# Performance work log

Measured on AMD Instinct MI355X. Metric: run time of the kernel, lower is better.

The kernel has to match this reference:

```python
import jax, jax.numpy as jnp
import numpy as np

N, C, H, W = 8, 512, 56, 56
CI = 256  # inter_channels = in_channels // reduction


def setup_inputs() -> dict:
    key = jax.random.key(0)
    ks = jax.random.split(key, 9)
    std = 0.01
    return {
        "x": jax.random.normal(ks[0], (N, C, H, W), dtype=jnp.float32),
        "W_g": jax.random.normal(ks[1], (CI, C), dtype=jnp.float32) * std,
        "b_g": jnp.zeros((CI,), dtype=jnp.float32),
        "W_theta": jax.random.normal(ks[2], (CI, C), dtype=jnp.float32) * std,
        "b_theta": jnp.zeros((CI,), dtype=jnp.float32),
        "W_phi": jax.random.normal(ks[3], (CI, C), dtype=jnp.float32) * std,
        "b_phi": jnp.zeros((CI,), dtype=jnp.float32),
        "W_out": jax.random.normal(ks[4], (C, CI), dtype=jnp.float32) * std,
        "b_out": jax.random.normal(ks[5], (C,), dtype=jnp.float32) * std,
    }


def _proj(Wt, b, xf):
    # 1x1 conv == channel GEMM over flattened spatial positions: (n, o, L)
    return jnp.einsum('oc,ncl->nol', Wt, xf) + b[None, :, None]


def reference(x, W_g, b_g, W_theta, b_theta, W_phi, b_phi, W_out, b_out):
    n, c, h, w = x.shape
    L = h * w
    xf = x.reshape(n, c, L)

    g_x = _proj(W_g, b_g, xf).transpose(0, 2, 1)          # (n, L, ci)
    theta_x = _proj(W_theta, b_theta, xf).transpose(0, 2, 1)  # (n, L, ci)
    phi_x = _proj(W_phi, b_phi, xf)                        # (n, ci, L)

    ci = theta_x.shape[-1]
    # embedded_gaussian with use_scale=True
    pairwise = jnp.einsum('nqc,nck->nqk', theta_x, phi_x) / jnp.sqrt(
        jnp.asarray(ci, dtype=x.dtype))
    pairwise = jax.nn.softmax(pairwise, axis=-1)           # (n, L, L)

    y = jnp.einsum('nqk,nkc->nqc', pairwise, g_x)          # (n, L, ci)
    y = y.transpose(0, 2, 1)                               # (n, ci, L)
    out = _proj(W_out, b_out, y).reshape(n, c, h, w)
    return x + out
```

## Files before the change

kernel.cpp:

```cpp
#include <hip/hip_runtime.h>
#include <stdint.h>

#define NB 8
#define CC 512
#define LL 3136
#define CIN 256

typedef __attribute__((ext_vector_type(8))) short bf8;
typedef __attribute__((ext_vector_type(4))) float f4;
typedef __attribute__((ext_vector_type(16))) float f16v;

__device__ __forceinline__ f4 mfma_bf16(bf8 a, bf8 b, f4 c) {
  return __builtin_amdgcn_mfma_f32_16x16x32_bf16(a, b, c, 0, 0, 0);
}

__device__ __forceinline__ f16v mfma32(bf8 a, bf8 b, f16v c) {
  return __builtin_amdgcn_mfma_f32_32x32x16_bf16(a, b, c, 0, 0, 0);
}

__device__ __forceinline__ unsigned short f2bf(float f) {
  unsigned int u = __float_as_uint(f);
  u += 0x7FFFu + ((u >> 16) & 1u);
  return (unsigned short)(u >> 16);
}

__device__ __forceinline__ void gload_lds16(const unsigned short* g, unsigned short* l) {
  __builtin_amdgcn_global_load_lds(
      (const __attribute__((address_space(1))) void*)g,
      (__attribute__((address_space(3))) void*)l, 16, 0, 0);
}

__global__ void k_convw(const float* Wth, const float* Wph, const float* Wg, const float* Wout,
                        unsigned short* dst) {
  int i = blockIdx.x * 256 + threadIdx.x;
  int which = i >> 17;
  int off = i & 131071;
  const float* s = which == 0 ? Wth : which == 1 ? Wph : which == 2 ? Wg : Wout;
  dst[i] = f2bf(s[off]);
}

__global__ __launch_bounds__(256) void k_xT(const float* x, unsigned short* xT) {
  __shared__ unsigned short tile[64][66];
  const int lt = blockIdx.x, n = blockIdx.y, ct = blockIdx.z;
  const int t = threadIdx.x;
  const float* xb = x + (size_t)n * CC * LL + (size_t)(ct * 64) * LL + lt * 64;
  const int tl = t & 63, trow = t >> 6;
#pragma unroll
  for (int i = 0; i < 16; ++i) {
    int c = i * 4 + trow;
    tile[c][tl] = f2bf(xb[(size_t)c * LL + tl]);
  }
  __syncthreads();
  unsigned short* xo = xT + (size_t)n * LL * CC + (size_t)(lt * 64) * CC + ct * 64;
  const int tc = t & 63, lrow = t >> 6;
#pragma unroll
  for (int i = 0; i < 16; ++i) {
    int l = i * 4 + lrow;
    xo[(size_t)l * CC + tc] = tile[tc][l];
  }
}

__global__ __launch_bounds__(256, 3) void k_proj(const unsigned short* Wbf,
    const float* bth, const float* bph, const float* bg,
    const unsigned short* xT, unsigned short* QT, unsigned short* KT, unsigned short* Vb) {
  __shared__ unsigned short wtile[2][8192];
  __shared__ unsigned short xtile[2][4096];
  const int bid = blockIdx.x;
  const int n = bid & 7, t = bid >> 3;
  const int lt = t % 49, z = t / 49;
  const int proj = z >> 1, cith = z & 1;
  const int tid = threadIdx.x;
  const int wave = tid >> 6, lane = tid & 63;
  const int quad = lane >> 4, c16 = lane & 15;

  const unsigned short* Wg = Wbf + proj * 131072 + (size_t)(cith * 128) * CC;
  const unsigned short* Xg = xT + (size_t)n * LL * CC + (size_t)(lt * 64) * CC;

  auto issue = [&](int chunk, int b) {
    const int cb = chunk * 64;
#pragma unroll
    for (int i = 0; i < 4; ++i) {
      int seg = i * 4 + wave;
      int p = seg * 64 + lane;
      int r = p >> 3, sl = p & 7, g = sl ^ (r & 7);
      gload_lds16(Wg + (size_t)r * CC + cb + g * 8, &wtile[b][seg * 512]);
    }
#pragma unroll
    for (int i = 0; i < 2; ++i) {
      int seg = i * 4 + wave;
      int p = seg * 64 + lane;
      int r = p >> 3, sl = p & 7, g = sl ^ (r & 7);
      gload_lds16(Xg + (size_t)r * CC + cb + g * 8, &xtile[b][seg * 512]);
    }
  };

  const f4 zz = {0.f, 0.f, 0.f, 0.f};
  f4 acc[2][4];
#pragma unroll
  for (int i = 0; i < 2; ++i)
#pragma unroll
    for (int j = 0; j < 4; ++j) acc[i][j] = zz;

  issue(0, 0);
  for (int chunk = 0; chunk < 8; ++chunk) {
    __syncthreads();
    if (chunk + 1 < 8) issue(chunk + 1, (chunk + 1) & 1);
    const int bb = chunk & 1;
#pragma unroll
    for (int kc = 0; kc < 2; ++kc) {
      const int slot = (kc * 4 + quad) ^ (c16 & 7);
      bf8 wf[2], xf[4];
#pragma unroll
      for (int sub = 0; sub < 2; ++sub)
        wf[sub] = *(const bf8*)(&wtile[bb][(wave * 32 + sub * 16 + c16) * 64 + slot * 8]);
#pragma unroll
      for (int nt = 0; nt < 4; ++nt)
        xf[nt] = *(const bf8*)(&xtile[bb][(nt * 16 + c16) * 64 + slot * 8]);
      if (proj < 2) {
#pragma unroll
        for (int sub = 0; sub < 2; ++sub)
#pragma unroll
          for (int nt = 0; nt < 4; ++nt)
            acc[sub][nt] = mfma_bf16(wf[sub], xf[nt], acc[sub][nt]);
      } else {
#pragma unroll
        for (int sub = 0; sub < 2; ++sub)
#pragma unroll
          for (int nt = 0; nt < 4; ++nt)
            acc[sub][nt] = mfma_bf16(xf[nt], wf[sub], acc[sub][nt]);
      }
    }
  }

  if (proj < 2) {
    const float* bias = proj == 0 ? bth : bph;
    unsigned short* dst = proj == 0 ? QT : KT;
#pragma unroll
    for (int sub = 0; sub < 2; ++sub) {
      const int ciB = cith * 128 + wave * 32 + sub * 16 + quad * 4;
      const float b0 = bias[ciB + 0], b1 = bias[ciB + 1];
      const float b2 = bias[ciB + 2], b3 = bias[ciB + 3];
#pragma unroll
      for (int nt = 0; nt < 4; ++nt) {
        int l = lt * 64 + nt * 16 + c16;
        ushort4 v;
        v.x = f2bf(acc[sub][nt][0] + b0);
        v.y = f2bf(acc[sub][nt][1] + b1);
        v.z = f2bf(acc[sub][nt][2] + b2);
        v.w = f2bf(acc[sub][nt][3] + b3);
        *(ushort4*)(dst + ((size_t)n * LL + l) * CIN + ciB) = v;
      }
    }
  } else {
#pragma unroll
    for (int sub = 0; sub < 2; ++sub) {
      const int ci = cith * 128 + wave * 32 + sub * 16 + c16;
      const float bv = bg[ci];
#pragma unroll
      for (int nt = 0; nt < 4; ++nt) {
        int l = lt * 64 + nt * 16 + quad * 4;
        ushort4 v;
        v.x = f2bf(acc[sub][nt][0] + bv);
        v.y = f2bf(acc[sub][nt][1] + bv);
        v.z = f2bf(acc[sub][nt][2] + bv);
        v.w = f2bf(acc[sub][nt][3] + bv);
        *(ushort4*)(Vb + ((size_t)n * CIN + ci) * LL + l) = v;
      }
    }
  }
}

__global__ __launch_bounds__(256, 2) void k_attn(const unsigned short* QT, const unsigned short* KT,
                                                 const unsigned short* Vb, unsigned short* Opart,
                                                 float* denp) {
  __shared__ unsigned short kbuf[2][8192];
  __shared__ unsigned short vbuf[2][8192];
  __shared__ __align__(16) unsigned short plds[4][1280];
  const int bid = blockIdx.x;
  const int n = bid & 7, ks = (bid >> 3) & 1, qb = bid >> 4;
  const int tid = threadIdx.x;
  const int wave = tid >> 6, lane = tid & 63;
  const int l31 = lane & 31, half = lane >> 5;
  int q0 = qb * 128 + wave * 32;
  const bool do_store = q0 < LL;
  if (q0 > LL - 32) q0 = LL - 32;
  const unsigned short* Qb = QT + ((size_t)n * LL + q0) * CIN;
  const unsigned short* Kks = KT + (size_t)n * LL * CIN + (size_t)(ks * 49 * 32) * CIN;
  const unsigned short* Vks = Vb + (size_t)n * CIN * LL + ks * 49 * 32;

  const float qs = 0.09016844005556021f;
  bf8 qf[16];
#pragma unroll
  for (int kc = 0; kc < 16; ++kc) {
    bf8 q = *(const bf8*)(Qb + (size_t)l31 * CIN + kc * 16 + half * 8);
#pragma unroll
    for (int e = 0; e < 8; ++e) {
      float f = __uint_as_float(((unsigned)(unsigned short)q[e]) << 16) * qs;
      q[e] = (short)f2bf(f);
    }
    qf[kc] = q;
  }

  f16v o[8];
#pragma unroll
  for (int t = 0; t < 8; ++t)
#pragma unroll
    for (int r = 0; r < 16; ++r) o[t][r] = 0.f;
  float sden = 0.f;

  auto issue = [&](int kt, int b) {
    const int k0 = kt * 32;
    const unsigned short* Kg = Kks + (size_t)k0 * CIN;
    const unsigned short* Vg = Vks + k0;
#pragma unroll
    for (int i = 0; i < 4; ++i) {
      int seg = i * 4 + wave;
      int idx = seg * 64 + lane;
      {
        int r = idx >> 5, sl = idx & 31, g = sl ^ r;
        gload_lds16(Kg + r * CIN + g * 8, &kbuf[b][seg * 512]);
      }
      {
        int r = idx >> 2, sl = idx & 3, g = sl ^ ((r >> 1) & 3);
        gload_lds16(Vg + (size_t)r * LL + g * 8, &vbuf[b][seg * 512]);
      }
    }
  };

  unsigned short* pw = &plds[wave][0];
  issue(0, 0);
  for (int kt = 0; kt < 49; ++kt) {
    __syncthreads();
    if (kt + 1 < 49) issue(kt + 1, (kt + 1) & 1);
    const int b = kt & 1;
    const unsigned short* kb = &kbuf[b][0];
    const unsigned short* vbp = &vbuf[b][0];

    f16v sc;
#pragma unroll
    for (int r = 0; r < 16; ++r) sc[r] = 0.f;
#pragma unroll
    for (int kc = 0; kc < 16; ++kc) {
      int slot = (kc * 2 + half) ^ l31;
      bf8 bfr = *(const bf8*)(kb + l31 * 256 + slot * 8);
      sc = mfma32(qf[kc], bfr, sc);
    }
#pragma unroll
    for (int r = 0; r < 16; ++r) {
      float p = __builtin_amdgcn_exp2f(sc[r]);
      int row = (r & 3) + 8 * (r >> 2) + 4 * half;
      pw[row * 40 + l31] = f2bf(p);
    }
    bf8 af[2];
#pragma unroll
    for (int kc2 = 0; kc2 < 2; ++kc2) {
      af[kc2] = *(const bf8*)(pw + l31 * 40 + kc2 * 16 + half * 8);
#pragma unroll
      for (int e = 0; e < 8; ++e)
        sden += __uint_as_float(((unsigned)(unsigned short)af[kc2][e]) << 16);
    }
#pragma unroll
    for (int t = 0; t < 8; ++t) {
#pragma unroll
      for (int kc2 = 0; kc2 < 2; ++kc2) {
        int slot = (kc2 * 2 + half) ^ ((l31 >> 1) & 3);
        bf8 v = *(const bf8*)(vbp + (t * 32 + l31) * 32 + slot * 8);
        o[t] = mfma32(af[kc2], v, o[t]);
      }
    }
  }

  sden += __shfl_xor(sden, 32);

  if (do_store) {
    if (lane < 32) denp[((size_t)ks * NB + n) * LL + q0 + l31] = sden;
    unsigned short* Ob = Opart + (((size_t)ks * NB + n) * LL + q0) * CIN;
#pragma unroll
    for (int t = 0; t < 8; ++t)
#pragma unroll
      for (int r = 0; r < 16; ++r) {
        int row = (r & 3) + 8 * (r >> 2) + 4 * half;
        Ob[(size_t)row * CIN + t * 32 + l31] = f2bf(o[t][r]);
      }
  }
}

__global__ void k_den(const float* denp, float* invden) {
  int i = blockIdx.x * 256 + threadIdx.x;
  if (i < NB * LL) invden[i] = 1.f / (denp[i] + denp[NB * LL + i]);
}

__global__ __launch_bounds__(256, 3) void k_out(const unsigned short* O0, const unsigned short* O1,
    const unsigned short* Wo, const float* bout, const float* invden,
    const float* x, float* out) {
  __shared__ unsigned short wtile[2][8192];
  __shared__ unsigned short otile[2][4096];
  const int bid = blockIdx.x;
  const int n = bid & 7, t = bid >> 3;
  const int lt = t % 49, cth = t / 49;
  const int tid = threadIdx.x;
  const int wave = tid >> 6, lane = tid & 63;
  const int quad = lane >> 4, c16 = lane & 15;

  const unsigned short* Wg = Wo + (size_t)(cth * 128) * CIN;
  const unsigned short* Og0 = O0 + ((size_t)n * LL + lt * 64) * CIN;
  const unsigned short* Og1 = O1 + ((size_t)n * LL + lt * 64) * CIN;

  auto issue = [&](int chunk, int b) {
    const int cb = (chunk & 3) * 64;
    const unsigned short* Og = chunk < 4 ? Og0 : Og1;
#pragma unroll
    for (int i = 0; i < 4; ++i) {
      int seg = i * 4 + wave;
      int p = seg * 64 + lane;
      int r = p >> 3, sl = p & 7, g = sl ^ (r & 7);
      gload_lds16(Wg + (size_t)r * CIN + cb + g * 8, &wtile[b][seg * 512]);
    }
#pragma unroll
    for (int i = 0; i < 2; ++i) {
      int seg = i * 4 + wave;
      int p = seg * 64 + lane;
      int r = p >> 3, sl = p & 7, g = sl ^ (r & 7);
      gload_lds16(Og + (size_t)r * CIN + cb + g * 8, &otile[b][seg * 512]);
    }
  };

  const f4 zz = {0.f, 0.f, 0.f, 0.f};
  f4 acc[4][2];
#pragma unroll
  for (int i = 0; i < 4; ++i)
#pragma unroll
    for (int j = 0; j < 2; ++j) acc[i][j] = zz;

  issue(0, 0);
  for (int chunk = 0; chunk < 8; ++chunk) {
    __syncthreads();
    if (chunk + 1 < 8) issue(chunk + 1, (chunk + 1) & 1);
    const int bb = chunk & 1;
#pragma unroll
    for (int kc = 0; kc < 2; ++kc) {
      const int slot = (kc * 4 + quad) ^ (c16 & 7);
      bf8 wf[2], ofr[4];
#pragma unroll
      for (int sub = 0; sub < 2; ++sub)
        wf[sub] = *(const bf8*)(&wtile[bb][(wave * 32 + sub * 16 + c16) * 64 + slot * 8]);
#pragma unroll
      for (int nt = 0; nt < 4; ++nt)
        ofr[nt] = *(const bf8*)(&otile[bb][(nt * 16 + c16) * 64 + slot * 8]);
#pragma unroll
      for (int nt = 0; nt < 4; ++nt)
#pragma unroll
        for (int sub = 0; sub < 2; ++sub)
          acc[nt][sub] = mfma_bf16(ofr[nt], wf[sub], acc[nt][sub]);
    }
  }

#pragma unroll
  for (int sub = 0; sub < 2; ++sub) {
    const int c = cth * 128 + wave * 32 + sub * 16 + c16;
    const float bv = bout[c];
#pragma unroll
    for (int nt = 0; nt < 4; ++nt) {
      int l = lt * 64 + nt * 16 + quad * 4;
      f4 iv = *(const f4*)(invden + (size_t)n * LL + l);
      size_t base = ((size_t)n * CC + c) * LL + l;
      f4 xv = *(const f4*)(x + base);
      f4 r;
      r[0] = xv[0] + bv + acc[nt][sub][0] * iv[0];
      r[1] = xv[1] + bv + acc[nt][sub][1] * iv[1];
      r[2] = xv[2] + bv + acc[nt][sub][2] * iv[2];
      r[3] = xv[3] + bv + acc[nt][sub][3] * iv[3];
      *(f4*)(out + base) = r;
    }
  }
}

extern "C" void kernel_launch(void* const* d_in, const int* in_sizes, int n_in,
                              void* d_out, int out_size, void* d_ws, size_t ws_size,
                              hipStream_t stream) {
  const float* x     = (const float*)d_in[0];
  const float* W_g   = (const float*)d_in[1];
  const float* b_g   = (const float*)d_in[2];
  const float* W_th  = (const float*)d_in[3];
  const float* b_th  = (const float*)d_in[4];
  const float* W_ph  = (const float*)d_in[5];
  const float* b_ph  = (const float*)d_in[6];
  const float* W_out = (const float*)d_in[7];
  const float* b_out = (const float*)d_in[8];

  char* ws = (char*)d_ws;
  const size_t SZ_W  = 1048576;
  const size_t SZ_P  = 12845056;
  unsigned short* Wbf = (unsigned short*)(ws);
  unsigned short* QT  = (unsigned short*)(ws + SZ_W);
  unsigned short* KT  = (unsigned short*)(ws + SZ_W + SZ_P);
  unsigned short* Vb  = (unsigned short*)(ws + SZ_W + 2 * SZ_P);
  unsigned short* xT  = (unsigned short*)(ws + SZ_W + 3 * SZ_P);
  unsigned short* O0  = xT;
  unsigned short* O1  = (unsigned short*)(ws + SZ_W + 4 * SZ_P);
  float* denp   = (float*)(ws + SZ_W + 5 * SZ_P);
  float* invden = (float*)(ws + SZ_W + 5 * SZ_P + 2 * NB * LL * 4);
  float* out = (float*)d_out;

  k_convw<<<2048, 256, 0, stream>>>(W_th, W_ph, W_g, W_out, Wbf);
  k_xT<<<dim3(49, 8, 8), 256, 0, stream>>>(x, xT);
  k_proj<<<2352, 256, 0, stream>>>(Wbf, b_th, b_ph, b_g, xT, QT, KT, Vb);
  k_attn<<<400, 256, 0, stream>>>(QT, KT, Vb, O0, denp);
  k_den<<<98, 256, 0, stream>>>(denp, invden);
  k_out<<<1568, 256, 0, stream>>>(O0, O1, Wbf + 3 * 131072, b_out, invden, x, out);
}
```

Before: 306.3 us.

## Compute S^T and build P operand in registers via permlane32 swap, dropping LDS staging

The QK^T MFMA now takes the operands in swapped order, so scores come out transposed, and the accumulation is split across two independent accumulators to shorten the MFMA dependency chain. The exp values are packed to bf16 with v_cvt_pk_bf16_f32, and v_permlane32_swap rearranges them directly into the A-operand layout for the PV MFMA. This removes the per-tile LDS write/read round trip of P and the per-wave plds buffer. The row-sum denominator is now taken from the fp32 probabilities rather than the bf16-rounded ones, which slightly changes the numerics.

Measured after the change: 335.1 us. 1.09x slower.

```diff
diff --git a/kernel.cpp b/kernel.cpp
--- a/kernel.cpp
+++ b/kernel.cpp
@@ -9,6 +9,7 @@
 typedef __attribute__((ext_vector_type(8))) short bf8;
 typedef __attribute__((ext_vector_type(4))) float f4;
 typedef __attribute__((ext_vector_type(16))) float f16v;
+typedef __attribute__((ext_vector_type(4))) int i4;
 
 __device__ __forceinline__ f4 mfma_bf16(bf8 a, bf8 b, f4 c) {
   return __builtin_amdgcn_mfma_f32_16x16x32_bf16(a, b, c, 0, 0, 0);
@@ -22,6 +23,12 @@
   unsigned int u = __float_as_uint(f);
   u += 0x7FFFu + ((u >> 16) & 1u);
   return (unsigned short)(u >> 16);
+}
+
+__device__ __forceinline__ int cvtpk_bf16(float lo, float hi) {
+  int r;
+  asm("v_cvt_pk_bf16_f32 %0, %1, %2" : "=v"(r) : "v"(lo), "v"(hi));
+  return r;
 }
 
 __device__ __forceinline__ void gload_lds16(const unsigned short* g, unsigned short* l) {
@@ -175,7 +182,6 @@
                                                  float* denp) {
   __shared__ unsigned short kbuf[2][8192];
   __shared__ unsigned short vbuf[2][8192];
-  __shared__ __align__(16) unsigned short plds[4][1280];
   const int bid = blockIdx.x;
   const int n = bid & 7, ks = (bid >> 3) & 1, qb = bid >> 4;
   const int tid = threadIdx.x;
@@ -227,7 +233,6 @@
     }
   };
 
-  unsigned short* pw = &plds[wave][0];
   issue(0, 0);
   for (int kt = 0; kt < 49; ++kt) {
     __syncthreads();
@@ -236,29 +241,45 @@
     const unsigned short* kb = &kbuf[b][0];
     const unsigned short* vbp = &vbuf[b][0];
 
-    f16v sc;
-#pragma unroll
-    for (int r = 0; r < 16; ++r) sc[r] = 0.f;
-#pragma unroll
-    for (int kc = 0; kc < 16; ++kc) {
-      int slot = (kc * 2 + half) ^ l31;
-      bf8 bfr = *(const bf8*)(kb + l31 * 256 + slot * 8);
-      sc = mfma32(qf[kc], bfr, sc);
-    }
-#pragma unroll
-    for (int r = 0; r < 16; ++r) {
-      float p = __builtin_amdgcn_exp2f(sc[r]);
-      int row = (r & 3) + 8 * (r >> 2) + 4 * half;
-      pw[row * 40 + l31] = f2bf(p);
-    }
+    f16v sc0, sc1;
+#pragma unroll
+    for (int r = 0; r < 16; ++r) { sc0[r] = 0.f; sc1[r] = 0.f; }
+#pragma unroll
+    for (int kc = 0; kc < 16; kc += 2) {
+      int slot0 = (kc * 2 + half) ^ l31;
+      int slot1 = ((kc + 1) * 2 + half) ^ l31;
+      bf8 kf0 = *(const bf8*)(kb + l31 * 256 + slot0 * 8);
+      bf8 kf1 = *(const bf8*)(kb + l31 * 256 + slot1 * 8);
+      sc0 = mfma32(kf0, qf[kc], sc0);
+      sc1 = mfma32(kf1, qf[kc + 1], sc1);
+    }
+
+    float p[16];
+#pragma unroll
+    for (int r = 0; r < 16; ++r)
+      p[r] = __builtin_amdgcn_exp2f(sc0[r] + sc1[r]);
+    {
+      float s0 = (p[0] + p[1]) + (p[2] + p[3]);
+      float s1 = (p[4] + p[5]) + (p[6] + p[7]);
+      float s2 = (p[8] + p[9]) + (p[10] + p[11]);
+      float s3 = (p[12] + p[13]) + (p[14] + p[15]);
+      sden += (s0 + s1) + (s2 + s3);
+    }
+
     bf8 af[2];
 #pragma unroll
-    for (int kc2 = 0; kc2 < 2; ++kc2) {
-      af[kc2] = *(const bf8*)(pw + l31 * 40 + kc2 * 16 + half * 8);
-#pragma unroll
-      for (int e = 0; e < 8; ++e)
-        sden += __uint_as_float(((unsigned)(unsigned short)af[kc2][e]) << 16);
-    }
+    for (int m = 0; m < 2; ++m) {
+      int x0 = cvtpk_bf16(p[8 * m + 0], p[8 * m + 1]);
+      int y0 = cvtpk_bf16(p[8 * m + 4], p[8 * m + 5]);
+      int x1 = cvtpk_bf16(p[8 * m + 2], p[8 * m + 3]);
+      int y1 = cvtpk_bf16(p[8 * m + 6], p[8 * m + 7]);
+      asm("v_permlane32_swap_b32 %0, %1" : "+v"(x0), "+v"(y0));
+      asm("v_permlane32_swap_b32 %0, %1" : "+v"(x1), "+v"(y1));
+      i4 w;
+      w[0] = x0; w[1] = x1; w[2] = y0; w[3] = y1;
+      af[m] = *(bf8*)&w;
+    }
+
 #pragma unroll
     for (int t = 0; t < 8; ++t) {
 #pragma unroll
```

## Build P operand in registers via transposed QK and permlane swap, dropping LDS

Applied to the files above, without the earlier changes.

The score MFMA now runs with K as the A operand and Q as B, so the score tile comes out transposed. Each lane then packs its exp2 probabilities to bf16 with v_cvt_pk_bf16_f32 and exchanges halves with v_permlane32_swap to form the PV A-operand directly in registers. This removes the per-tile LDS write and read of P, the plds buffer, and the reconstruction of the denominator from bf16 values. The denominator is now summed from fp32 probabilities rather than rounded bf16, which changes numerics slightly, and correctness depends on the lane mapping of the permlane swap.

Measured after the change: 294.3 us. 1.04x faster.

```diff
diff --git a/kernel.cpp b/kernel.cpp
--- a/kernel.cpp
+++ b/kernel.cpp
@@ -9,6 +9,7 @@
 typedef __attribute__((ext_vector_type(8))) short bf8;
 typedef __attribute__((ext_vector_type(4))) float f4;
 typedef __attribute__((ext_vector_type(16))) float f16v;
+typedef __attribute__((ext_vector_type(4))) int i4;
 
 __device__ __forceinline__ f4 mfma_bf16(bf8 a, bf8 b, f4 c) {
   return __builtin_amdgcn_mfma_f32_16x16x32_bf16(a, b, c, 0, 0, 0);
@@ -22,6 +23,12 @@
   unsigned int u = __float_as_uint(f);
   u += 0x7FFFu + ((u >> 16) & 1u);
   return (unsigned short)(u >> 16);
+}
+
+__device__ __forceinline__ int cvtpk_bf16(float lo, float hi) {
+  int r;
+  asm("v_cvt_pk_bf16_f32 %0, %1, %2" : "=v"(r) : "v"(lo), "v"(hi));
+  return r;
 }
 
 __device__ __forceinline__ void gload_lds16(const unsigned short* g, unsigned short* l) {
@@ -175,7 +182,6 @@
                                                  float* denp) {
   __shared__ unsigned short kbuf[2][8192];
   __shared__ unsigned short vbuf[2][8192];
-  __shared__ __align__(16) unsigned short plds[4][1280];
   const int bid = blockIdx.x;
   const int n = bid & 7, ks = (bid >> 3) & 1, qb = bid >> 4;
   const int tid = threadIdx.x;
@@ -227,7 +233,6 @@
     }
   };
 
-  unsigned short* pw = &plds[wave][0];
   issue(0, 0);
   for (int kt = 0; kt < 49; ++kt) {
     __syncthreads();
@@ -242,23 +247,33 @@
 #pragma unroll
     for (int kc = 0; kc < 16; ++kc) {
       int slot = (kc * 2 + half) ^ l31;
-      bf8 bfr = *(const bf8*)(kb + l31 * 256 + slot * 8);
-      sc = mfma32(qf[kc], bfr, sc);
-    }
-#pragma unroll
-    for (int r = 0; r < 16; ++r) {
-      float p = __builtin_amdgcn_exp2f(sc[r]);
-      int row = (r & 3) + 8 * (r >> 2) + 4 * half;
-      pw[row * 40 + l31] = f2bf(p);
-    }
+      bf8 kf = *(const bf8*)(kb + l31 * 256 + slot * 8);
+      sc = mfma32(kf, qf[kc], sc);
+    }
+
     bf8 af[2];
 #pragma unroll
-    for (int kc2 = 0; kc2 < 2; ++kc2) {
-      af[kc2] = *(const bf8*)(pw + l31 * 40 + kc2 * 16 + half * 8);
-#pragma unroll
-      for (int e = 0; e < 8; ++e)
-        sden += __uint_as_float(((unsigned)(unsigned short)af[kc2][e]) << 16);
-    }
+    for (int m = 0; m < 2; ++m) {
+      float p0 = __builtin_amdgcn_exp2f(sc[8 * m + 0]);
+      float p1 = __builtin_amdgcn_exp2f(sc[8 * m + 1]);
+      float p2 = __builtin_amdgcn_exp2f(sc[8 * m + 2]);
+      float p3 = __builtin_amdgcn_exp2f(sc[8 * m + 3]);
+      float p4 = __builtin_amdgcn_exp2f(sc[8 * m + 4]);
+      float p5 = __builtin_amdgcn_exp2f(sc[8 * m + 5]);
+      float p6 = __builtin_amdgcn_exp2f(sc[8 * m + 6]);
+      float p7 = __builtin_amdgcn_exp2f(sc[8 * m + 7]);
+      sden += ((p0 + p1) + (p2 + p3)) + ((p4 + p5) + (p6 + p7));
+      int x0 = cvtpk_bf16(p0, p1);
+      int y0 = cvtpk_bf16(p4, p5);
+      int x1 = cvtpk_bf16(p2, p3);
+      int y1 = cvtpk_bf16(p6, p7);
+      asm("v_permlane32_swap_b32 %0, %1" : "+v"(x0), "+v"(y0));
+      asm("v_permlane32_swap_b32 %0, %1" : "+v"(x1), "+v"(y1));
+      i4 w;
+      w[0] = x0; w[1] = x1; w[2] = y0; w[3] = y1;
+      af[m] = *(bf8*)&w;
+    }
+
 #pragma unroll
     for (int t = 0; t < 8; ++t) {
 #pragma unroll
```
